# Kernel tuning notes

Hardware: AMD Instinct MI355X
Metric: run time of the kernel (lower is better)

## Reference

```python
import jax, jax.numpy as jnp
import numpy as np

NOISE_SCALE = 0.1  # init_kwargs['noise_scale']


def setup_inputs() -> dict:
    key = jax.random.key(0)
    k_x, k_b, k_e, k_p = jax.random.split(key, 4)
    B, F, NB = 65536, 256, 16
    x = jax.random.normal(k_x, (B, F), dtype=jnp.float32)
    # per-feature sorted bin edges spanning roughly the data range [-3, 3]
    bins = jnp.sort(jax.random.uniform(k_b, (F, NB + 1), dtype=jnp.float32,
                                       minval=-3.0, maxval=3.0), axis=1)
    eps = jax.random.normal(k_e, (B, F), dtype=jnp.float32)  # stands in for torch.randn per bin
    noise_params = jnp.zeros((F * NB,), dtype=jnp.float32)   # nn.Parameter init = zeros
    return {"x": x, "bins": bins, "eps": eps, "noise_params": noise_params}


def reference(x, bins, eps, noise_params):
    B, F = x.shape
    params = noise_params.reshape(F, -1)           # [F, n_bins]
    n_bins = params.shape[1]
    # bucketize: for each feature i, idx such that bins[i, idx] <= x < bins[i, idx+1]
    # searchsorted(side='right') returns count of edges <= v; subtract 1 -> bin index
    idx = jax.vmap(lambda b, v: jnp.searchsorted(b, v, side='right'),
                   in_axes=(0, 1), out_axes=1)(bins, x) - 1   # [B, F]
    valid = (idx >= 0) & (idx < n_bins)            # values outside edges get no noise
    jc = jnp.clip(idx, 0, n_bins - 1)
    # gather per-(sample, feature) noise scale: params[feature, bin]
    scale = jax.nn.sigmoid(params[jnp.arange(F)[None, :], jc])  # [B, F]
    noise = jnp.where(valid, eps * scale * NOISE_SCALE, 0.0)
    return x + noise
```

## Files before the change

### kernel.cpp

```cpp
#include <hip/hip_runtime.h>


#define NFEAT 256
#define NBINS 16
#define NEDGE 17
#define NOISE_SCALE 0.1f

__global__ __launch_bounds__(256) void noise_learn_kernel(
    const float* __restrict__ x,
    const float* __restrict__ bins,
    const float* __restrict__ eps,
    const float* __restrict__ params,
    float* __restrict__ out,
    int total4)
{
    __shared__ float s_bins[NEDGE][NFEAT];
    __shared__ float s_scale[NBINS][NFEAT];

    const int t = threadIdx.x;

    #pragma unroll
    for (int e = 0; e < NEDGE; ++e)
        s_bins[e][t] = bins[t * NEDGE + e];

    #pragma unroll
    for (int k = 0; k < NBINS; ++k) {
        float p = params[t * NBINS + k];
        s_scale[k][t] = 1.0f / (1.0f + expf(-p));
    }
    __syncthreads();

    const int gid = blockIdx.x * 256 + t;
    const int stride = gridDim.x * 256;
    const int fbase = (gid & 63) * 4;

    for (int g = gid; g < total4; g += stride) {
        const float4 xv = reinterpret_cast<const float4*>(x)[g];
        const float4 ev = reinterpret_cast<const float4*>(eps)[g];

        int c0 = 0, c1 = 0, c2 = 0, c3 = 0;
        #pragma unroll
        for (int e = 0; e < NEDGE; ++e) {
            const float4 be = *reinterpret_cast<const float4*>(&s_bins[e][fbase]);
            c0 += (be.x <= xv.x) ? 1 : 0;
            c1 += (be.y <= xv.y) ? 1 : 0;
            c2 += (be.z <= xv.z) ? 1 : 0;
            c3 += (be.w <= xv.w) ? 1 : 0;
        }

        float4 ov;
        {
            const int idx = c0 - 1;
            const int jc = idx < 0 ? 0 : (idx > NBINS - 1 ? NBINS - 1 : idx);
            const float sc = s_scale[jc][fbase + 0];
            ov.x = xv.x + ((idx >= 0 && idx < NBINS) ? ev.x * sc * NOISE_SCALE : 0.0f);
        }
        {
            const int idx = c1 - 1;
            const int jc = idx < 0 ? 0 : (idx > NBINS - 1 ? NBINS - 1 : idx);
            const float sc = s_scale[jc][fbase + 1];
            ov.y = xv.y + ((idx >= 0 && idx < NBINS) ? ev.y * sc * NOISE_SCALE : 0.0f);
        }
        {
            const int idx = c2 - 1;
            const int jc = idx < 0 ? 0 : (idx > NBINS - 1 ? NBINS - 1 : idx);
            const float sc = s_scale[jc][fbase + 2];
            ov.z = xv.z + ((idx >= 0 && idx < NBINS) ? ev.z * sc * NOISE_SCALE : 0.0f);
        }
        {
            const int idx = c3 - 1;
            const int jc = idx < 0 ? 0 : (idx > NBINS - 1 ? NBINS - 1 : idx);
            const float sc = s_scale[jc][fbase + 3];
            ov.w = xv.w + ((idx >= 0 && idx < NBINS) ? ev.w * sc * NOISE_SCALE : 0.0f);
        }

        reinterpret_cast<float4*>(out)[g] = ov;
    }
}

extern "C" void kernel_launch(void* const* d_in, const int* in_sizes, int n_in,
                              void* d_out, int out_size, void* d_ws, size_t ws_size,
                              hipStream_t stream) {
    const float* x      = (const float*)d_in[0];
    const float* bins   = (const float*)d_in[1];
    const float* eps    = (const float*)d_in[2];
    const float* params = (const float*)d_in[3];
    float* out = (float*)d_out;

    const int total4 = out_size / 4;
    dim3 block(256);
    dim3 grid(2048);
    noise_learn_kernel<<<grid, block, 0, stream>>>(x, bins, eps, params, out, total4);
}
```

Measured before the change: 40.80 us.

## Hold per-feature bin edges in registers and process float2 per thread

Each thread now handles two features via float2 loads. The 17 bin edges for each of those features are loaded once into registers instead of being re-read from shared memory on every iteration. Shared memory is merged into one buffer reused for edges and then sigmoid scales, which lowers LDS footprint, and launch bounds request 8 blocks per CU. The trade-off is narrower global accesses, twice as many loop iterations, and higher register pressure from the 34 edge registers.

After: 43.36 us. +6.3%, slower.

```diff
diff --git a/kernel.cpp b/kernel.cpp
--- a/kernel.cpp
+++ b/kernel.cpp
@@ -6,75 +6,69 @@
 #define NEDGE 17
 #define NOISE_SCALE 0.1f
 
-__global__ __launch_bounds__(256) void noise_learn_kernel(
+__global__ __launch_bounds__(256, 8) void noise_learn_kernel(
     const float* __restrict__ x,
     const float* __restrict__ bins,
     const float* __restrict__ eps,
     const float* __restrict__ params,
     float* __restrict__ out,
-    int total4)
+    int total2)
 {
-    __shared__ float s_bins[NEDGE][NFEAT];
-    __shared__ float s_scale[NBINS][NFEAT];
+    __shared__ float s_mem[NEDGE * NFEAT];
 
     const int t = threadIdx.x;
 
     #pragma unroll
-    for (int e = 0; e < NEDGE; ++e)
-        s_bins[e][t] = bins[t * NEDGE + e];
+    for (int i = t; i < NEDGE * NFEAT; i += 256)
+        s_mem[i] = bins[i];
+    __syncthreads();
+
+    const int gid = blockIdx.x * 256 + t;
+    const int f0 = (gid & 127) * 2;
+    const int f1 = f0 + 1;
+
+    float e0[NEDGE], e1[NEDGE];
+    #pragma unroll
+    for (int e = 0; e < NEDGE; ++e) {
+        e0[e] = s_mem[f0 * NEDGE + e];
+        e1[e] = s_mem[f1 * NEDGE + e];
+    }
+    __syncthreads();
 
     #pragma unroll
     for (int k = 0; k < NBINS; ++k) {
         float p = params[t * NBINS + k];
-        s_scale[k][t] = 1.0f / (1.0f + expf(-p));
+        s_mem[k * NFEAT + t] = 1.0f / (1.0f + expf(-p));
     }
     __syncthreads();
 
-    const int gid = blockIdx.x * 256 + t;
     const int stride = gridDim.x * 256;
-    const int fbase = (gid & 63) * 4;
+    for (int g = gid; g < total2; g += stride) {
+        const float2 xv = reinterpret_cast<const float2*>(x)[g];
+        const float2 ev = reinterpret_cast<const float2*>(eps)[g];
 
-    for (int g = gid; g < total4; g += stride) {
-        const float4 xv = reinterpret_cast<const float4*>(x)[g];
-        const float4 ev = reinterpret_cast<const float4*>(eps)[g];
-
-        int c0 = 0, c1 = 0, c2 = 0, c3 = 0;
+        int c0 = 0, c1 = 0;
         #pragma unroll
         for (int e = 0; e < NEDGE; ++e) {
-            const float4 be = *reinterpret_cast<const float4*>(&s_bins[e][fbase]);
-            c0 += (be.x <= xv.x) ? 1 : 0;
-            c1 += (be.y <= xv.y) ? 1 : 0;
-            c2 += (be.z <= xv.z) ? 1 : 0;
-            c3 += (be.w <= xv.w) ? 1 : 0;
+            c0 += (e0[e] <= xv.x) ? 1 : 0;
+            c1 += (e1[e] <= xv.y) ? 1 : 0;
         }
 
-        float4 ov;
+        float2 ov;
         {
             const int idx = c0 - 1;
             const int jc = idx < 0 ? 0 : (idx > NBINS - 1 ? NBINS - 1 : idx);
-            const float sc = s_scale[jc][fbase + 0];
-            ov.x = xv.x + ((idx >= 0 && idx < NBINS) ? ev.x * sc * NOISE_SCALE : 0.0f);
+            const float sc = s_mem[jc * NFEAT + f0];
+            ov.x = xv.x + (((unsigned)idx < (unsigned)NBINS) ? ev.x * sc * NOISE_SCALE : 0.0f);
         }
         {
             const int idx = c1 - 1;
             const int jc = idx < 0 ? 0 : (idx > NBINS - 1 ? NBINS - 1 : idx);
-            const float sc = s_scale[jc][fbase + 1];
-            ov.y = xv.y + ((idx >= 0 && idx < NBINS) ? ev.y * sc * NOISE_SCALE : 0.0f);
-        }
-        {
-            const int idx = c2 - 1;
-            const int jc = idx < 0 ? 0 : (idx > NBINS - 1 ? NBINS - 1 : idx);
-            const float sc = s_scale[jc][fbase + 2];
-            ov.z = xv.z + ((idx >= 0 && idx < NBINS) ? ev.z * sc * NOISE_SCALE : 0.0f);
-        }
-        {
-            const int idx = c3 - 1;
-            const int jc = idx < 0 ? 0 : (idx > NBINS - 1 ? NBINS - 1 : idx);
-            const float sc = s_scale[jc][fbase + 3];
-            ov.w = xv.w + ((idx >= 0 && idx < NBINS) ? ev.w * sc * NOISE_SCALE : 0.0f);
+            const float sc = s_mem[jc * NFEAT + f1];
+            ov.y = xv.y + (((unsigned)idx < (unsigned)NBINS) ? ev.y * sc * NOISE_SCALE : 0.0f);
         }
 
-        reinterpret_cast<float4*>(out)[g] = ov;
+        reinterpret_cast<float2*>(out)[g] = ov;
     }
 }
 
@@ -87,8 +81,8 @@
     const float* params = (const float*)d_in[3];
     float* out = (float*)d_out;
 
-    const int total4 = out_size / 4;
+    const int total2 = out_size / 2;
     dim3 block(256);
     dim3 grid(2048);
-    noise_learn_kernel<<<grid, block, 0, stream>>>(x, bins, eps, params, out, total4);
+    noise_learn_kernel<<<grid, block, 0, stream>>>(x, bins, eps, params, out, total2);
 }
```

## Hold per-thread bin edges in registers and share one padded LDS buffer

Applied to the files above, without the earlier changes.

Each thread now loads its four features' 17 bin edges into registers once, so the per-element loop compares against registers instead of reading LDS. The LDS staging is coalesced, a single buffer is reused for edges and then for the padded sigmoid table to avoid bank conflicts, and __expf replaces expf. This raises register pressure to about 68 extra VGPRs, with launch bounds set to 4 blocks per CU. It also adds an extra barrier in the prologue.

After: 53.37 us. 30.8% more time.

```diff
diff --git a/kernel.cpp b/kernel.cpp
--- a/kernel.cpp
+++ b/kernel.cpp
@@ -4,9 +4,10 @@
 #define NFEAT 256
 #define NBINS 16
 #define NEDGE 17
+#define SPAD  257
 #define NOISE_SCALE 0.1f
 
-__global__ __launch_bounds__(256) void noise_learn_kernel(
+__global__ __launch_bounds__(256, 4) void noise_learn_kernel(
     const float* __restrict__ x,
     const float* __restrict__ bins,
     const float* __restrict__ eps,
@@ -14,25 +15,35 @@
     float* __restrict__ out,
     int total4)
 {
-    __shared__ float s_bins[NEDGE][NFEAT];
-    __shared__ float s_scale[NBINS][NFEAT];
+    __shared__ float s_mem[NEDGE * NFEAT];
 
     const int t = threadIdx.x;
 
     #pragma unroll
-    for (int e = 0; e < NEDGE; ++e)
-        s_bins[e][t] = bins[t * NEDGE + e];
+    for (int i = t; i < NEDGE * NFEAT; i += 256)
+        s_mem[i] = bins[i];
+    __syncthreads();
+
+    const int f0 = (t & 63) * 4;
+    float e[4][NEDGE];
+    #pragma unroll
+    for (int j = 0; j < 4; ++j)
+        #pragma unroll
+        for (int i = 0; i < NEDGE; ++i)
+            e[j][i] = s_mem[(f0 + j) * NEDGE + i];
+    __syncthreads();
 
     #pragma unroll
-    for (int k = 0; k < NBINS; ++k) {
-        float p = params[t * NBINS + k];
-        s_scale[k][t] = 1.0f / (1.0f + expf(-p));
+    for (int i = t; i < NFEAT * NBINS; i += 256) {
+        const float p = params[i];
+        const int f = i >> 4;
+        const int k = i & (NBINS - 1);
+        s_mem[k * SPAD + f] = 1.0f / (1.0f + __expf(-p));
     }
     __syncthreads();
 
     const int gid = blockIdx.x * 256 + t;
     const int stride = gridDim.x * 256;
-    const int fbase = (gid & 63) * 4;
 
     for (int g = gid; g < total4; g += stride) {
         const float4 xv = reinterpret_cast<const float4*>(x)[g];
@@ -40,38 +51,37 @@
 
         int c0 = 0, c1 = 0, c2 = 0, c3 = 0;
         #pragma unroll
-        for (int e = 0; e < NEDGE; ++e) {
-            const float4 be = *reinterpret_cast<const float4*>(&s_bins[e][fbase]);
-            c0 += (be.x <= xv.x) ? 1 : 0;
-            c1 += (be.y <= xv.y) ? 1 : 0;
-            c2 += (be.z <= xv.z) ? 1 : 0;
-            c3 += (be.w <= xv.w) ? 1 : 0;
+        for (int i = 0; i < NEDGE; ++i) {
+            c0 += (e[0][i] <= xv.x) ? 1 : 0;
+            c1 += (e[1][i] <= xv.y) ? 1 : 0;
+            c2 += (e[2][i] <= xv.z) ? 1 : 0;
+            c3 += (e[3][i] <= xv.w) ? 1 : 0;
         }
 
         float4 ov;
         {
             const int idx = c0 - 1;
             const int jc = idx < 0 ? 0 : (idx > NBINS - 1 ? NBINS - 1 : idx);
-            const float sc = s_scale[jc][fbase + 0];
-            ov.x = xv.x + ((idx >= 0 && idx < NBINS) ? ev.x * sc * NOISE_SCALE : 0.0f);
+            const float sc = s_mem[jc * SPAD + f0 + 0];
+            ov.x = xv.x + (((unsigned)idx < (unsigned)NBINS) ? ev.x * sc * NOISE_SCALE : 0.0f);
         }
         {
             const int idx = c1 - 1;
             const int jc = idx < 0 ? 0 : (idx > NBINS - 1 ? NBINS - 1 : idx);
-            const float sc = s_scale[jc][fbase + 1];
-            ov.y = xv.y + ((idx >= 0 && idx < NBINS) ? ev.y * sc * NOISE_SCALE : 0.0f);
+            const float sc = s_mem[jc * SPAD + f0 + 1];
+            ov.y = xv.y + (((unsigned)idx < (unsigned)NBINS) ? ev.y * sc * NOISE_SCALE : 0.0f);
         }
         {
             const int idx = c2 - 1;
             const int jc = idx < 0 ? 0 : (idx > NBINS - 1 ? NBINS - 1 : idx);
-            const float sc = s_scale[jc][fbase + 2];
-            ov.z = xv.z + ((idx >= 0 && idx < NBINS) ? ev.z * sc * NOISE_SCALE : 0.0f);
+            const float sc = s_mem[jc * SPAD + f0 + 2];
+            ov.z = xv.z + (((unsigned)idx < (unsigned)NBINS) ? ev.z * sc * NOISE_SCALE : 0.0f);
         }
         {
             const int idx = c3 - 1;
             const int jc = idx < 0 ? 0 : (idx > NBINS - 1 ? NBINS - 1 : idx);
-            const float sc = s_scale[jc][fbase + 3];
-            ov.w = xv.w + ((idx >= 0 && idx < NBINS) ? ev.w * sc * NOISE_SCALE : 0.0f);
+            const float sc = s_mem[jc * SPAD + f0 + 3];
+            ov.w = xv.w + (((unsigned)idx < (unsigned)NBINS) ? ev.w * sc * NOISE_SCALE : 0.0f);
         }
 
         reinterpret_cast<float4*>(out)[g] = ov;
```
